# Kernel tuning notes

Measured on AMD Instinct MI355X. Metric: run time of the kernel, lower is better.

Reference implementation:

```python
import jax, jax.numpy as jnp
import numpy as np

B, S, D = 2, 2048, 2048
NH, NKV, DH = 16, 4, 128
NG = NH // NKV  # query heads per kv head


def rope_apply(x, cos, sin):
    # x: [B, H, S, DH]; cos/sin: [S, DH//2]
    x1, x2 = jnp.split(x, 2, axis=-1)
    c = cos[None, None, :, :]
    s = sin[None, None, :, :]
    return jnp.concatenate([x1 * c - x2 * s, x1 * s + x2 * c], axis=-1)


def setup_inputs() -> dict:
    key = jax.random.key(0)
    ks = jax.random.split(key, 6)
    x = jax.random.normal(ks[0], (B, S, D), dtype=jnp.float32)
    # real RoPE frequencies
    inv_freq = 1.0 / (10000.0 ** (jnp.arange(0, DH // 2, dtype=jnp.float32) * 2.0 / DH))
    angles = jnp.arange(S, dtype=jnp.float32)[:, None] * inv_freq[None, :]  # [S, DH//2]
    cos, sin = jnp.cos(angles), jnp.sin(angles)
    mask = jnp.tril(jnp.ones((S, S), dtype=bool))[None, None]  # causal [1,1,S,S]
    sc = 0.02
    Wq = jax.random.normal(ks[1], (D, NH * DH), dtype=jnp.float32) * sc
    Wk = jax.random.normal(ks[2], (D, NKV * DH), dtype=jnp.float32) * sc
    Wv = jax.random.normal(ks[3], (D, NKV * DH), dtype=jnp.float32) * sc
    Wo = jax.random.normal(ks[4], (NH * DH, D), dtype=jnp.float32) * sc
    return {"x": x, "cos": cos, "sin": sin, "mask": mask,
            "Wq": Wq, "Wk": Wk, "Wv": Wv, "Wo": Wo}


def reference(x, cos, sin, mask, Wq, Wk, Wv, Wo):
    b, s, _ = x.shape
    q = (x @ Wq).reshape(b, s, NH, DH).transpose(0, 2, 1, 3)    # [B,NH,S,DH]
    k = (x @ Wk).reshape(b, s, NKV, DH).transpose(0, 2, 1, 3)   # [B,NKV,S,DH]
    v = (x @ Wv).reshape(b, s, NKV, DH).transpose(0, 2, 1, 3)
    q = rope_apply(q, cos, sin)
    k = rope_apply(k, cos, sin)
    new_kv_cache = (k, v)
    k_exp = jnp.repeat(k, NG, axis=1)  # [B,NH,S,DH]
    v_exp = jnp.repeat(v, NG, axis=1)
    scale = jnp.float32(np.sqrt(DH))
    scores = jnp.einsum('bhqd,bhkd->bhqk', q, k_exp) / scale
    scores = jnp.where(mask, scores, jnp.float32(-1e9))
    weights = jax.nn.softmax(scores, axis=-1)
    context = jnp.einsum('bhqk,bhkd->bhqd', weights, v_exp)
    context = context.transpose(0, 2, 1, 3).reshape(b, s, NH * DH)
    output = context @ Wo
    return output, new_kv_cache[0], new_kv_cache[1]
```

## Files before the change

### kernel.cpp

```cpp
#include <hip/hip_runtime.h>
#include <stdint.h>

#define Bb 2
#define Ss 2048
#define Dd 2048
#define NHh 16
#define NKVv 4
#define DHh 128
#define Mm_ (Bb*Ss)
#define NQq (NHh*DHh)

using bf16x8 = __attribute__((ext_vector_type(8))) __bf16;
using f32x4  = __attribute__((ext_vector_type(4))) float;

__device__ __forceinline__ unsigned short f2bf(float f) {
  unsigned u = __float_as_uint(f);
  u += 0x7fffu + ((u >> 16) & 1u);
  return (unsigned short)(u >> 16);
}
__device__ __forceinline__ float bf2f(unsigned short s) {
  return __uint_as_float(((unsigned)s) << 16);
}

__global__ void k_convert(const float* __restrict__ in, unsigned short* __restrict__ out, int n4) {
  const int i = blockIdx.x * blockDim.x + threadIdx.x;
  if (i >= n4) return;
  const float4 v = ((const float4*)in)[i];
  ushort4 o;
  o.x = f2bf(v.x); o.y = f2bf(v.y); o.z = f2bf(v.z); o.w = f2bf(v.w);
  ((ushort4*)out)[i] = o;
}

__global__ __launch_bounds__(256) void k_transpose(const float* __restrict__ in,
                                                   unsigned short* __restrict__ out,
                                                   int Kk, int Nn) {
  __shared__ float tile[32][33];
  const int n0 = blockIdx.x * 32, k0 = blockIdx.y * 32;
  const int tx = threadIdx.x & 31, ty = threadIdx.x >> 5;
  #pragma unroll
  for (int i = 0; i < 4; ++i)
    tile[ty + i * 8][tx] = in[(size_t)(k0 + ty + i * 8) * Nn + n0 + tx];
  __syncthreads();
  #pragma unroll
  for (int i = 0; i < 4; ++i)
    out[(size_t)(n0 + ty + i * 8) * Kk + k0 + tx] = f2bf(tile[tx][ty + i * 8]);
}

template<int BNW, int MODE>
__global__ __launch_bounds__(512) void k_gemm256(const unsigned short* __restrict__ A,
                                                 const unsigned short* __restrict__ BT,
                                                 int Kdim,
                                                 unsigned short* __restrict__ Qo,
                                                 float* __restrict__ kfo,
                                                 float* __restrict__ outV,
                                                 unsigned short* __restrict__ vTb,
                                                 float* __restrict__ Cf) {
  __shared__ unsigned short ldsA[2][16384];
  __shared__ unsigned short ldsB[2][4096 * BNW];
  const int tid = threadIdx.x;
  const int lane = tid & 63;
  const int lg = lane >> 4, ll = lane & 15;
  const int wid = tid >> 6;
  const int wm = wid >> 2, wn = wid & 3;
  const int m0 = blockIdx.y << 8;
  const int n0 = blockIdx.x * (64 * BNW);

  f32x4 acc[8][BNW] = {};
  bf16x8 bfr[BNW];

  auto stage_A = [&](int buf, int kt, int s) {
    const int c = (s << 9) + tid;
    const int row = c >> 3, c16 = c & 7;
    const int csrc = (c16 ^ (row & 7)) << 3;
    const unsigned short* src = A + (size_t)(m0 + row) * Kdim + kt * 64 + csrc;
    __builtin_amdgcn_global_load_lds(
        (const __attribute__((address_space(1))) void*)src,
        (__attribute__((address_space(3))) void*)(&ldsA[buf][0] + c * 8), 16, 0, 0);
  };
  auto stage_B = [&](int buf, int kt, int s) {
    const int c = (s << 9) + tid;
    const int row = c >> 3, c16 = c & 7;
    const int csrc = (c16 ^ (row & 7)) << 3;
    const unsigned short* src = BT + (size_t)(n0 + row) * Kdim + kt * 64 + csrc;
    __builtin_amdgcn_global_load_lds(
        (const __attribute__((address_space(1))) void*)src,
        (__attribute__((address_space(3))) void*)(&ldsB[buf][0] + c * 8), 16, 0, 0);
  };

  #pragma unroll
  for (int s = 0; s < 4; ++s) stage_A(0, 0, s);
  #pragma unroll
  for (int s = 0; s < BNW; ++s) stage_B(0, 0, s);
  __syncthreads();

  const int nkt = Kdim >> 6;
  int cur = 0;
  for (int kt = 0; kt < nkt; ++kt) {
    const int nxt = cur ^ 1;
    const bool hn = (kt + 1 < nkt);
    const char* Atl = (const char*)&ldsA[cur][0];
    const char* Btl = (const char*)&ldsB[cur][0];

    auto rdB = [&](int ks) {
      #pragma unroll
      for (int i = 0; i < BNW; ++i) {
        const int r = wn * (16 * BNW) + i * 16 + ll;
        bfr[i] = *(const bf16x8*)(const void*)(
            Btl + r * 128 + ((ks * 64 + lg * 16) ^ ((r & 7) << 4)));
      }
    };
    auto quad = [&](int mh, int ks) {
      bf16x8 af[4];
      #pragma unroll
      for (int i = 0; i < 4; ++i) {
        const int r = wm * 128 + (mh * 4 + i) * 16 + ll;
        af[i] = *(const bf16x8*)(const void*)(
            Atl + r * 128 + ((ks * 64 + lg * 16) ^ ((r & 7) << 4)));
      }
      __builtin_amdgcn_s_setprio(1);
      #pragma unroll
      for (int i = 0; i < 4; ++i)
        #pragma unroll
        for (int n = 0; n < BNW; ++n)
          acc[mh * 4 + i][n] =
              __builtin_amdgcn_mfma_f32_16x16x32_bf16(af[i], bfr[n], acc[mh * 4 + i][n], 0, 0, 0);
      __builtin_amdgcn_s_setprio(0);
    };

    rdB(0);
    if (hn) { stage_A(nxt, kt + 1, 0); stage_A(nxt, kt + 1, 1);
              stage_A(nxt, kt + 1, 2); stage_A(nxt, kt + 1, 3); }
    __builtin_amdgcn_s_barrier();
    quad(0, 0);
    __builtin_amdgcn_s_barrier();
    if (hn) {
      #pragma unroll
      for (int s = 0; s < BNW; ++s) stage_B(nxt, kt + 1, s);
    }
    __builtin_amdgcn_s_barrier();
    quad(1, 0);
    __builtin_amdgcn_s_barrier();
    rdB(1);
    __builtin_amdgcn_s_barrier();
    quad(0, 1);
    __builtin_amdgcn_s_barrier();
    quad(1, 1);
    if (hn) {
      asm volatile("s_waitcnt vmcnt(0)" ::: "memory");
    }
    __builtin_amdgcn_s_barrier();
    cur ^= 1;
  }

  #pragma unroll
  for (int mi = 0; mi < 8; ++mi)
    #pragma unroll
    for (int ni = 0; ni < BNW; ++ni) {
      const int row4 = m0 + wm * 128 + mi * 16 + lg * 4;
      const int col = n0 + wn * (16 * BNW) + ni * 16 + ll;
      if (MODE == 1) {
        #pragma unroll
        for (int jj = 0; jj < 4; ++jj)
          Cf[(size_t)(row4 + jj) * 2048 + col] = acc[mi][ni][jj];
      } else {
        if (col < 2048) {
          #pragma unroll
          for (int jj = 0; jj < 4; ++jj)
            Qo[(size_t)(row4 + jj) * 2048 + col] = f2bf(acc[mi][ni][jj]);
        } else if (col < 2560) {
          #pragma unroll
          for (int jj = 0; jj < 4; ++jj)
            kfo[(size_t)(row4 + jj) * 512 + (col - 2048)] = acc[mi][ni][jj];
        } else {
          const int kv = (col - 2560) >> 7, dh = (col - 2560) & 127;
          const int b = row4 >> 11, s0 = row4 & 2047;
          #pragma unroll
          for (int jj = 0; jj < 4; ++jj)
            outV[((size_t)(b * NKVv + kv) * Ss + s0 + jj) * DHh + dh] = acc[mi][ni][jj];
          ushort4 pk;
          pk.x = f2bf(acc[mi][ni][0]); pk.y = f2bf(acc[mi][ni][1]);
          pk.z = f2bf(acc[mi][ni][2]); pk.w = f2bf(acc[mi][ni][3]);
          *(ushort4*)&vTb[((size_t)(b * NKVv + kv) * DHh + dh) * Ss + s0] = pk;
        }
      }
    }
}

__global__ void k_rope_k(const float* __restrict__ kf, const float* __restrict__ cosT,
                         const float* __restrict__ sinT, float* __restrict__ outK,
                         unsigned short* __restrict__ kbb) {
  const int idx = blockIdx.x * blockDim.x + threadIdx.x;
  if (idx >= Mm_ * NKVv * 64) return;
  const int dh2 = idx & 63;
  const int kv = (idx >> 6) & 3;
  const int m = idx >> 8;
  const int s = m & (Ss - 1);
  const int b = m >> 11;
  const size_t src = (size_t)m * 512 + kv * DHh + dh2;
  const float x1 = kf[src], x2 = kf[src + 64];
  const float c = cosT[s * 64 + dh2], sn = sinT[s * 64 + dh2];
  const float o1 = x1 * c - x2 * sn, o2 = x1 * sn + x2 * c;
  const size_t dst = ((size_t)(b * NKVv + kv) * Ss + s) * DHh + dh2;
  outK[dst] = o1; outK[dst + 64] = o2;
  kbb[dst] = f2bf(o1); kbb[dst + 64] = f2bf(o2);
}

__global__ __launch_bounds__(256) void k_attn(const unsigned short* __restrict__ qb,
                                              const unsigned short* __restrict__ kb,
                                              const unsigned short* __restrict__ vT,
                                              const float* __restrict__ cosT,
                                              const float* __restrict__ sinT,
                                              unsigned short* __restrict__ ctxb) {
  const int linear = blockIdx.y * 32 + blockIdx.x;
  const int r = linear >> 8;
  const int u = linear & 255;
  const int q2 = u & 7;
  const int bh = u >> 3;
  int qt;
  if      (r == 0) qt = q2;
  else if (r == 1) qt = 15 - q2;
  else if (r == 2) qt = 16 + q2;
  else             qt = 31 - q2;

  const int b = bh >> 4, h = bh & 15;
  const int kvh = h >> 2;
  const int tid = threadIdx.x, wid = tid >> 6, lane = tid & 63;
  const int lg = lane >> 4, ll = lane & 15;
  __shared__ unsigned short kts[8192];
  __shared__ unsigned short vts[8192];
  __shared__ unsigned short p_s[4096];
  const char* ktc = (const char*)kts;
  const char* vtc = (const char*)vts;
  char* pwc = (char*)p_s + wid * 2048;
  const int swz = (ll & 7) << 4;
  const unsigned short* kbase = kb + (size_t)(b * NKVv + kvh) * Ss * DHh;
  const unsigned short* vbase = vT + (size_t)(b * NKVv + kvh) * DHh * Ss;
  const int qrow_f = qt * 64 + wid * 16 + ll;
  const unsigned short* qrow = qb + (size_t)(b * Ss + qrow_f) * NQq + h * DHh;

  uint4 rq[4];
  #pragma unroll
  for (int ks = 0; ks < 4; ++ks)
    rq[ks] = *(const uint4*)(const void*)(qrow + ks * 32 + lg * 8);
  bf16x8 qfr[4];
  {
    const unsigned short* rqs = (const unsigned short*)rq;
    unsigned short qtmp[4][8];
    const float scq = 0.12751746595544662f;
    #pragma unroll
    for (int ksh = 0; ksh < 2; ++ksh) {
      #pragma unroll
      for (int e = 0; e < 8; ++e) {
        const int dh2 = ksh * 32 + lg * 8 + e;
        const float c = cosT[qrow_f * 64 + dh2], sn = sinT[qrow_f * 64 + dh2];
        const float x1 = bf2f(rqs[ksh * 8 + e]);
        const float x2 = bf2f(rqs[(ksh + 2) * 8 + e]);
        qtmp[ksh][e]     = f2bf((x1 * c - x2 * sn) * scq);
        qtmp[ksh + 2][e] = f2bf((x1 * sn + x2 * c) * scq);
      }
    }
    #pragma unroll
    for (int ks = 0; ks < 4; ++ks) qfr[ks] = *(const bf16x8*)(const void*)qtmp[ks];
  }

  union { unsigned int u4[4]; bf16x8 v; } onesu;
  onesu.u4[0] = onesu.u4[1] = onesu.u4[2] = onesu.u4[3] = 0x3F803F80u;
  const bf16x8 onesf = onesu.v;

  f32x4 ctx[9] = {};
  const int qr0 = qt * 64 + wid * 16 + lg * 4;
  const int nkt = qt + 1;

  auto stage_k = [&](int ktile) {
    #pragma unroll
    for (int i = 0; i < 4; ++i) {
      const int s = i * 256 + tid;
      const int krow = s >> 4, kcs = (s & 15) ^ (krow & 7);
      const unsigned short* ksrc = kbase + (size_t)(ktile * 64 + krow) * DHh + kcs * 8;
      __builtin_amdgcn_global_load_lds(
          (const __attribute__((address_space(1))) void*)ksrc,
          (__attribute__((address_space(3))) void*)(kts + (i * 256 + wid * 64) * 8), 16, 0, 0);
    }
  };
  auto stage_v = [&](int ktile) {
    #pragma unroll
    for (int i = 0; i < 4; ++i) {
      const int s = i * 256 + tid;
      const int vrow = s >> 3, vcs = (s & 7) ^ (vrow & 7);
      const unsigned short* vsrc = vbase + (size_t)vrow * Ss + ktile * 64 + vcs * 8;
      __builtin_amdgcn_global_load_lds(
          (const __attribute__((address_space(1))) void*)vsrc,
          (__attribute__((address_space(3))) void*)(vts + (i * 256 + wid * 64) * 8), 16, 0, 0);
    }
  };

  stage_k(0);
  __syncthreads();
  for (int kt = 0; kt < nkt; ++kt) {
    stage_v(kt);
    f32x4 sc[4] = {};
    __builtin_amdgcn_s_setprio(1);
    #pragma unroll
    for (int ks = 0; ks < 4; ++ks) {
      #pragma unroll
      for (int cb = 0; cb < 4; ++cb) {
        const bf16x8 kfr = *(const bf16x8*)(const void*)(
            ktc + ((cb * 16 + ll) << 8) + (((ks << 6) + (lg << 4)) ^ swz));
        sc[cb] = __builtin_amdgcn_mfma_f32_16x16x32_bf16(qfr[ks], kfr, sc[cb], 0, 0, 0);
      }
    }
    __builtin_amdgcn_s_setprio(0);
    const bool domask = (kt == qt);
    float pv[4][4];
    #pragma unroll
    for (int cb = 0; cb < 4; ++cb)
      #pragma unroll
      for (int j = 0; j < 4; ++j) {
        float s = sc[cb][j];
        if (domask && (kt * 64 + cb * 16 + ll > qr0 + j)) s = -1e30f;
        pv[cb][j] = exp2f(s - 8.656170245333781f);
      }
    #pragma unroll
    for (int cb = 0; cb < 4; ++cb)
      #pragma unroll
      for (int j = 0; j < 4; ++j) {
        const int prow = lg * 4 + j;
        *(unsigned short*)(pwc + (prow << 7) + (((cb << 5) + (ll << 1)) ^ ((prow & 7) << 4))) =
            (unsigned short)((__float_as_uint(pv[cb][j]) + 0x8000u) >> 16);
      }
    __syncthreads();
    if (kt + 1 < nkt) stage_k(kt + 1);
    __builtin_amdgcn_s_setprio(1);
    #pragma unroll
    for (int k2 = 0; k2 < 2; ++k2) {
      const bf16x8 pa = *(const bf16x8*)(const void*)(
          pwc + (ll << 7) + (((k2 << 6) + (lg << 4)) ^ swz));
      #pragma unroll
      for (int ob = 0; ob < 8; ++ob) {
        const bf16x8 vfr = *(const bf16x8*)(const void*)(
            vtc + ((ob * 16 + ll) << 7) + (((k2 << 6) + (lg << 4)) ^ swz));
        ctx[ob] = __builtin_amdgcn_mfma_f32_16x16x32_bf16(pa, vfr, ctx[ob], 0, 0, 0);
      }
      ctx[8] = __builtin_amdgcn_mfma_f32_16x16x32_bf16(pa, onesf, ctx[8], 0, 0, 0);
    }
    __builtin_amdgcn_s_setprio(0);
    __syncthreads();
  }
  #pragma unroll
  for (int j = 0; j < 4; ++j) {
    const float inv = 1.f / ctx[8][j];
    unsigned short* crow = ctxb + (size_t)(b * Ss + qr0 + j) * NQq + h * DHh;
    #pragma unroll
    for (int ob = 0; ob < 8; ++ob)
      crow[ob * 16 + ll] = f2bf(ctx[ob][j] * inv);
  }
}

extern "C" void kernel_launch(void* const* d_in, const int* in_sizes, int n_in,
                              void* d_out, int out_size, void* d_ws, size_t ws_size,
                              hipStream_t stream) {
  const float* x    = (const float*)d_in[0];
  const float* cosT = (const float*)d_in[1];
  const float* sinT = (const float*)d_in[2];
  const float* Wq   = (const float*)d_in[4];
  const float* Wk   = (const float*)d_in[5];
  const float* Wv   = (const float*)d_in[6];
  const float* Wo   = (const float*)d_in[7];
  float* out  = (float*)d_out;
  float* outK = out + (size_t)Mm_ * Dd;
  float* outV = outK + (size_t)Bb * NKVv * Ss * DHh;

  char* ws = (char*)d_ws;
  size_t off = 0;
  auto alloc = [&](size_t bytes) -> void* {
    void* p = ws + off;
    off += (bytes + 255) & ~(size_t)255;
    return p;
  };
  unsigned short* xb    = (unsigned short*)alloc((size_t)Mm_ * Dd * 2);
  unsigned short* wqkvT = (unsigned short*)alloc((size_t)3072 * Dd * 2);
  unsigned short* woT   = (unsigned short*)alloc((size_t)Dd * NQq * 2);
  unsigned short* qfb   = (unsigned short*)alloc((size_t)Mm_ * NQq * 2);
  float*          kf    = (float*)alloc((size_t)Mm_ * 512 * 4);
  unsigned short* kbb   = (unsigned short*)alloc((size_t)Bb * NKVv * Ss * DHh * 2);
  unsigned short* vTb   = (unsigned short*)alloc((size_t)Bb * NKVv * Ss * DHh * 2);
  unsigned short* ctxb  = (unsigned short*)alloc((size_t)Mm_ * NQq * 2);
  if (off > ws_size) return;

  k_convert<<<(Mm_ * Dd / 4 + 255) / 256, 256, 0, stream>>>(x, xb, Mm_ * Dd / 4);
  k_transpose<<<dim3(64, 64), 256, 0, stream>>>(Wq, wqkvT, Dd, Dd);
  k_transpose<<<dim3(16, 64), 256, 0, stream>>>(Wk, wqkvT + (size_t)2048 * Dd, Dd, 512);
  k_transpose<<<dim3(16, 64), 256, 0, stream>>>(Wv, wqkvT + (size_t)2560 * Dd, Dd, 512);
  k_transpose<<<dim3(64, 64), 256, 0, stream>>>(Wo, woT, Dd, Dd);
  k_gemm256<3, 0><<<dim3(16, 16), 512, 0, stream>>>(
      xb, wqkvT, Dd, qfb, kf, outV, vTb, (float*)nullptr);
  k_rope_k<<<(Mm_ * NKVv * 64 + 255) / 256, 256, 0, stream>>>(kf, cosT, sinT, outK, kbb);
  k_attn<<<dim3(32, 32), 256, 0, stream>>>(qfb, kbb, vTb, cosT, sinT, ctxb);
  k_gemm256<2, 1><<<dim3(16, 16), 512, 0, stream>>>(
      ctxb, woT, NQq, (unsigned short*)nullptr, (float*)nullptr,
      (float*)nullptr, (unsigned short*)nullptr, out);
}
```

Measured before the change: 204.9 us.

## Double attention query tile per block to reuse staged K/V tiles

Each attention block now handles 128 query rows instead of 64, with each wave computing two 16-row query blocks that share every K and V fragment read from LDS. The grid is halved and the causal tile scheduling is simplified to pair tiles qt and 15-qt. Waves whose rows are fully masked skip the last K tile. This aims to halve K/V global staging and LDS reads per query row, at the cost of more registers (two score and context accumulator sets), a larger P buffer in LDS, and fewer blocks to fill the GPU.

```diff
diff --git a/kernel.cpp b/kernel.cpp
--- a/kernel.cpp
+++ b/kernel.cpp
@@ -205,22 +205,18 @@
   kbb[dst] = f2bf(o1); kbb[dst + 64] = f2bf(o2);
 }
 
-__global__ __launch_bounds__(256) void k_attn(const unsigned short* __restrict__ qb,
-                                              const unsigned short* __restrict__ kb,
-                                              const unsigned short* __restrict__ vT,
-                                              const float* __restrict__ cosT,
-                                              const float* __restrict__ sinT,
-                                              unsigned short* __restrict__ ctxb) {
-  const int linear = blockIdx.y * 32 + blockIdx.x;
+__global__ __launch_bounds__(256, 2) void k_attn(const unsigned short* __restrict__ qb,
+                                                 const unsigned short* __restrict__ kb,
+                                                 const unsigned short* __restrict__ vT,
+                                                 const float* __restrict__ cosT,
+                                                 const float* __restrict__ sinT,
+                                                 unsigned short* __restrict__ ctxb) {
+  const int linear = blockIdx.y * 16 + blockIdx.x;
   const int r = linear >> 8;
   const int u = linear & 255;
-  const int q2 = u & 7;
+  const int q3 = u & 7;
   const int bh = u >> 3;
-  int qt;
-  if      (r == 0) qt = q2;
-  else if (r == 1) qt = 15 - q2;
-  else if (r == 2) qt = 16 + q2;
-  else             qt = 31 - q2;
+  const int qt = r ? (15 - q3) : q3;
 
   const int b = bh >> 4, h = bh & 15;
   const int kvh = h >> 2;
@@ -228,22 +224,24 @@
   const int lg = lane >> 4, ll = lane & 15;
   __shared__ unsigned short kts[8192];
   __shared__ unsigned short vts[8192];
-  __shared__ unsigned short p_s[4096];
+  __shared__ unsigned short p_s[16384];
   const char* ktc = (const char*)kts;
   const char* vtc = (const char*)vts;
-  char* pwc = (char*)p_s + wid * 2048;
+  char* pwc = (char*)p_s + wid * 8192;
   const int swz = (ll & 7) << 4;
   const unsigned short* kbase = kb + (size_t)(b * NKVv + kvh) * Ss * DHh;
   const unsigned short* vbase = vT + (size_t)(b * NKVv + kvh) * DHh * Ss;
-  const int qrow_f = qt * 64 + wid * 16 + ll;
-  const unsigned short* qrow = qb + (size_t)(b * Ss + qrow_f) * NQq + h * DHh;
-
-  uint4 rq[4];
-  #pragma unroll
-  for (int ks = 0; ks < 4; ++ks)
-    rq[ks] = *(const uint4*)(const void*)(qrow + ks * 32 + lg * 8);
-  bf16x8 qfr[4];
-  {
+  const int qbase = qt * 128 + wid * 32;
+
+  bf16x8 qfr[2][4];
+  #pragma unroll
+  for (int rb = 0; rb < 2; ++rb) {
+    const int qrow_f = qbase + rb * 16 + ll;
+    const unsigned short* qrow = qb + (size_t)(b * Ss + qrow_f) * NQq + h * DHh;
+    uint4 rq[4];
+    #pragma unroll
+    for (int ks = 0; ks < 4; ++ks)
+      rq[ks] = *(const uint4*)(const void*)(qrow + ks * 32 + lg * 8);
     const unsigned short* rqs = (const unsigned short*)rq;
     unsigned short qtmp[4][8];
     const float scq = 0.12751746595544662f;
@@ -260,16 +258,17 @@
       }
     }
     #pragma unroll
-    for (int ks = 0; ks < 4; ++ks) qfr[ks] = *(const bf16x8*)(const void*)qtmp[ks];
+    for (int ks = 0; ks < 4; ++ks) qfr[rb][ks] = *(const bf16x8*)(const void*)qtmp[ks];
   }
 
   union { unsigned int u4[4]; bf16x8 v; } onesu;
   onesu.u4[0] = onesu.u4[1] = onesu.u4[2] = onesu.u4[3] = 0x3F803F80u;
   const bf16x8 onesf = onesu.v;
 
-  f32x4 ctx[9] = {};
-  const int qr0 = qt * 64 + wid * 16 + lg * 4;
-  const int nkt = qt + 1;
+  f32x4 ctx[2][9] = {};
+  const int qr0a = qbase + lg * 4;
+  const int qr0b = qbase + 16 + lg * 4;
+  const int nkt = 2 * qt + 2;
 
   auto stage_k = [&](int ktile) {
     #pragma unroll
@@ -298,61 +297,74 @@
   __syncthreads();
   for (int kt = 0; kt < nkt; ++kt) {
     stage_v(kt);
-    f32x4 sc[4] = {};
-    __builtin_amdgcn_s_setprio(1);
-    #pragma unroll
-    for (int ks = 0; ks < 4; ++ks) {
-      #pragma unroll
-      for (int cb = 0; cb < 4; ++cb) {
-        const bf16x8 kfr = *(const bf16x8*)(const void*)(
-            ktc + ((cb * 16 + ll) << 8) + (((ks << 6) + (lg << 4)) ^ swz));
-        sc[cb] = __builtin_amdgcn_mfma_f32_16x16x32_bf16(qfr[ks], kfr, sc[cb], 0, 0, 0);
-      }
-    }
-    __builtin_amdgcn_s_setprio(0);
-    const bool domask = (kt == qt);
-    float pv[4][4];
-    #pragma unroll
-    for (int cb = 0; cb < 4; ++cb)
-      #pragma unroll
-      for (int j = 0; j < 4; ++j) {
-        float s = sc[cb][j];
-        if (domask && (kt * 64 + cb * 16 + ll > qr0 + j)) s = -1e30f;
-        pv[cb][j] = exp2f(s - 8.656170245333781f);
-      }
-    #pragma unroll
-    for (int cb = 0; cb < 4; ++cb)
-      #pragma unroll
-      for (int j = 0; j < 4; ++j) {
-        const int prow = lg * 4 + j;
-        *(unsigned short*)(pwc + (prow << 7) + (((cb << 5) + (ll << 1)) ^ ((prow & 7) << 4))) =
-            (unsigned short)((__float_as_uint(pv[cb][j]) + 0x8000u) >> 16);
-      }
+    const bool active = (wid >= 2) || (kt + 1 < nkt);
+    if (active) {
+      f32x4 sc[2][4] = {};
+      __builtin_amdgcn_s_setprio(1);
+      #pragma unroll
+      for (int ks = 0; ks < 4; ++ks) {
+        #pragma unroll
+        for (int cb = 0; cb < 4; ++cb) {
+          const bf16x8 kfr = *(const bf16x8*)(const void*)(
+              ktc + ((cb * 16 + ll) << 8) + (((ks << 6) + (lg << 4)) ^ swz));
+          sc[0][cb] = __builtin_amdgcn_mfma_f32_16x16x32_bf16(qfr[0][ks], kfr, sc[0][cb], 0, 0, 0);
+          sc[1][cb] = __builtin_amdgcn_mfma_f32_16x16x32_bf16(qfr[1][ks], kfr, sc[1][cb], 0, 0, 0);
+        }
+      }
+      __builtin_amdgcn_s_setprio(0);
+      #pragma unroll
+      for (int rb = 0; rb < 2; ++rb) {
+        const int qr0 = rb ? qr0b : qr0a;
+        const bool domask = ((kt + 1) << 6) > (qbase + rb * 16);
+        #pragma unroll
+        for (int cb = 0; cb < 4; ++cb)
+          #pragma unroll
+          for (int j = 0; j < 4; ++j) {
+            float s = sc[rb][cb][j];
+            if (domask && (kt * 64 + cb * 16 + ll > qr0 + j)) s = -1e30f;
+            const float p = exp2f(s - 8.656170245333781f);
+            const int prow = rb * 16 + lg * 4 + j;
+            *(unsigned short*)(pwc + (prow << 7) + (((cb << 5) + (ll << 1)) ^ ((prow & 7) << 4))) =
+                (unsigned short)((__float_as_uint(p) + 0x8000u) >> 16);
+          }
+      }
+    }
     __syncthreads();
     if (kt + 1 < nkt) stage_k(kt + 1);
-    __builtin_amdgcn_s_setprio(1);
-    #pragma unroll
-    for (int k2 = 0; k2 < 2; ++k2) {
-      const bf16x8 pa = *(const bf16x8*)(const void*)(
-          pwc + (ll << 7) + (((k2 << 6) + (lg << 4)) ^ swz));
-      #pragma unroll
-      for (int ob = 0; ob < 8; ++ob) {
-        const bf16x8 vfr = *(const bf16x8*)(const void*)(
-            vtc + ((ob * 16 + ll) << 7) + (((k2 << 6) + (lg << 4)) ^ swz));
-        ctx[ob] = __builtin_amdgcn_mfma_f32_16x16x32_bf16(pa, vfr, ctx[ob], 0, 0, 0);
-      }
-      ctx[8] = __builtin_amdgcn_mfma_f32_16x16x32_bf16(pa, onesf, ctx[8], 0, 0, 0);
-    }
-    __builtin_amdgcn_s_setprio(0);
+    if (active) {
+      __builtin_amdgcn_s_setprio(1);
+      #pragma unroll
+      for (int k2 = 0; k2 < 2; ++k2) {
+        bf16x8 pa[2];
+        #pragma unroll
+        for (int rb = 0; rb < 2; ++rb)
+          pa[rb] = *(const bf16x8*)(const void*)(
+              pwc + (((rb * 16 + ll)) << 7) + (((k2 << 6) + (lg << 4)) ^ swz));
+        #pragma unroll
+        for (int ob = 0; ob < 8; ++ob) {
+          const bf16x8 vfr = *(const bf16x8*)(const void*)(
+              vtc + ((ob * 16 + ll) << 7) + (((k2 << 6) + (lg << 4)) ^ swz));
+          ctx[0][ob] = __builtin_amdgcn_mfma_f32_16x16x32_bf16(pa[0], vfr, ctx[0][ob], 0, 0, 0);
+          ctx[1][ob] = __builtin_amdgcn_mfma_f32_16x16x32_bf16(pa[1], vfr, ctx[1][ob], 0, 0, 0);
+        }
+        ctx[0][8] = __builtin_amdgcn_mfma_f32_16x16x32_bf16(pa[0], onesf, ctx[0][8], 0, 0, 0);
+        ctx[1][8] = __builtin_amdgcn_mfma_f32_16x16x32_bf16(pa[1], onesf, ctx[1][8], 0, 0, 0);
+      }
+      __builtin_amdgcn_s_setprio(0);
+    }
     __syncthreads();
   }
   #pragma unroll
-  for (int j = 0; j < 4; ++j) {
-    const float inv = 1.f / ctx[8][j];
-    unsigned short* crow = ctxb + (size_t)(b * Ss + qr0 + j) * NQq + h * DHh;
-    #pragma unroll
-    for (int ob = 0; ob < 8; ++ob)
-      crow[ob * 16 + ll] = f2bf(ctx[ob][j] * inv);
+  for (int rb = 0; rb < 2; ++rb) {
+    const int qr0 = rb ? qr0b : qr0a;
+    #pragma unroll
+    for (int j = 0; j < 4; ++j) {
+      const float inv = 1.f / ctx[rb][8][j];
+      unsigned short* crow = ctxb + (size_t)(b * Ss + qr0 + j) * NQq + h * DHh;
+      #pragma unroll
+      for (int ob = 0; ob < 8; ++ob)
+        crow[ob * 16 + ll] = f2bf(ctx[rb][ob][j] * inv);
+    }
   }
 }
 
@@ -395,7 +407,7 @@
   k_gemm256<3, 0><<<dim3(16, 16), 512, 0, stream>>>(
       xb, wqkvT, Dd, qfb, kf, outV, vTb, (float*)nullptr);
   k_rope_k<<<(Mm_ * NKVv * 64 + 255) / 256, 256, 0, stream>>>(kf, cosT, sinT, outK, kbb);
-  k_attn<<<dim3(32, 32), 256, 0, stream>>>(qfb, kbb, vTb, cosT, sinT, ctxb);
+  k_attn<<<dim3(16, 32), 256, 0, stream>>>(qfb, kbb, vTb, cosT, sinT, ctxb);
   k_gemm256<2, 1><<<dim3(16, 16), 512, 0, stream>>>(
       ctxb, woT, NQq, (unsigned short*)nullptr, (float*)nullptr,
       (float*)nullptr, (unsigned short*)nullptr, out);
```

After: 209.1 us. +2.1%, slower.

## Read K and V fragments directly from global memory instead of LDS staging

Applied to the files above, without the earlier changes.

The attention kernel no longer stages K and V tiles into shared memory with async global-to-LDS copies. Each wave now loads its MFMA operand fragments straight from global memory, which also drops the block-wide barriers around the staging. This aims to remove LDS traffic and synchronisation stalls. The cost is that all four waves fetch the same K/V tile independently, with strided 16-byte loads that rely on L1/L2 hits, and the software double-buffering of K is lost.

```diff
diff --git a/kernel.cpp b/kernel.cpp
--- a/kernel.cpp
+++ b/kernel.cpp
@@ -226,17 +226,13 @@
   const int kvh = h >> 2;
   const int tid = threadIdx.x, wid = tid >> 6, lane = tid & 63;
   const int lg = lane >> 4, ll = lane & 15;
-  __shared__ unsigned short kts[8192];
-  __shared__ unsigned short vts[8192];
   __shared__ unsigned short p_s[4096];
-  const char* ktc = (const char*)kts;
-  const char* vtc = (const char*)vts;
   char* pwc = (char*)p_s + wid * 2048;
-  const int swz = (ll & 7) << 4;
   const unsigned short* kbase = kb + (size_t)(b * NKVv + kvh) * Ss * DHh;
   const unsigned short* vbase = vT + (size_t)(b * NKVv + kvh) * DHh * Ss;
   const int qrow_f = qt * 64 + wid * 16 + ll;
   const unsigned short* qrow = qb + (size_t)(b * Ss + qrow_f) * NQq + h * DHh;
+  const int swz = (ll & 7) << 4;
 
   uint4 rq[4];
   #pragma unroll
@@ -271,33 +267,7 @@
   const int qr0 = qt * 64 + wid * 16 + lg * 4;
   const int nkt = qt + 1;
 
-  auto stage_k = [&](int ktile) {
-    #pragma unroll
-    for (int i = 0; i < 4; ++i) {
-      const int s = i * 256 + tid;
-      const int krow = s >> 4, kcs = (s & 15) ^ (krow & 7);
-      const unsigned short* ksrc = kbase + (size_t)(ktile * 64 + krow) * DHh + kcs * 8;
-      __builtin_amdgcn_global_load_lds(
-          (const __attribute__((address_space(1))) void*)ksrc,
-          (__attribute__((address_space(3))) void*)(kts + (i * 256 + wid * 64) * 8), 16, 0, 0);
-    }
-  };
-  auto stage_v = [&](int ktile) {
-    #pragma unroll
-    for (int i = 0; i < 4; ++i) {
-      const int s = i * 256 + tid;
-      const int vrow = s >> 3, vcs = (s & 7) ^ (vrow & 7);
-      const unsigned short* vsrc = vbase + (size_t)vrow * Ss + ktile * 64 + vcs * 8;
-      __builtin_amdgcn_global_load_lds(
-          (const __attribute__((address_space(1))) void*)vsrc,
-          (__attribute__((address_space(3))) void*)(vts + (i * 256 + wid * 64) * 8), 16, 0, 0);
-    }
-  };
-
-  stage_k(0);
-  __syncthreads();
   for (int kt = 0; kt < nkt; ++kt) {
-    stage_v(kt);
     f32x4 sc[4] = {};
     __builtin_amdgcn_s_setprio(1);
     #pragma unroll
@@ -305,7 +275,7 @@
       #pragma unroll
       for (int cb = 0; cb < 4; ++cb) {
         const bf16x8 kfr = *(const bf16x8*)(const void*)(
-            ktc + ((cb * 16 + ll) << 8) + (((ks << 6) + (lg << 4)) ^ swz));
+            kbase + (size_t)(kt * 64 + cb * 16 + ll) * DHh + ks * 32 + lg * 8);
         sc[cb] = __builtin_amdgcn_mfma_f32_16x16x32_bf16(qfr[ks], kfr, sc[cb], 0, 0, 0);
       }
     }
@@ -328,8 +298,6 @@
         *(unsigned short*)(pwc + (prow << 7) + (((cb << 5) + (ll << 1)) ^ ((prow & 7) << 4))) =
             (unsigned short)((__float_as_uint(pv[cb][j]) + 0x8000u) >> 16);
       }
-    __syncthreads();
-    if (kt + 1 < nkt) stage_k(kt + 1);
     __builtin_amdgcn_s_setprio(1);
     #pragma unroll
     for (int k2 = 0; k2 < 2; ++k2) {
@@ -338,13 +306,12 @@
       #pragma unroll
       for (int ob = 0; ob < 8; ++ob) {
         const bf16x8 vfr = *(const bf16x8*)(const void*)(
-            vtc + ((ob * 16 + ll) << 7) + (((k2 << 6) + (lg << 4)) ^ swz));
+            vbase + (size_t)(ob * 16 + ll) * Ss + kt * 64 + k2 * 32 + lg * 8);
         ctx[ob] = __builtin_amdgcn_mfma_f32_16x16x32_bf16(pa, vfr, ctx[ob], 0, 0, 0);
       }
       ctx[8] = __builtin_amdgcn_mfma_f32_16x16x32_bf16(pa, onesf, ctx[8], 0, 0, 0);
     }
     __builtin_amdgcn_s_setprio(0);
-    __syncthreads();
   }
   #pragma unroll
   for (int j = 0; j < 4; ++j) {
```

After: 391.4 us. 91.0% more time.
